# Kernel optimization log

Hardware: AMD Instinct MI355X
Metric: run time of the kernel (lower is better)

## Reference

```python
import jax, jax.numpy as jnp
import numpy as np

K = 3; PAD = 1; STRIDE = 1; EPS = 1e-5


def setup_inputs() -> dict:
    key = jax.random.key(0)
    k0, k1, k2 = jax.random.split(key, 3)
    B, C, H, W, O = 4, 256, 64, 64, 256
    x = jax.random.normal(k0, (B, C, H, W), jnp.float32)
    # offset conv: small random weights so offsets are nontrivial but bounded
    w_off = jax.random.normal(k1, (2 * K * K, C, K, K), jnp.float32) * 0.01
    b_off = jnp.zeros((2 * K * K,), jnp.float32)
    # kaiming normal, mode=fan_out: std = sqrt(2 / (O*K*K))
    w_def = jax.random.normal(k2, (O, C, K, K), jnp.float32) * np.float32(np.sqrt(2.0 / (O * K * K)))
    gamma = jnp.ones((O,), jnp.float32)
    beta = jnp.zeros((O,), jnp.float32)
    return {"x": x, "w_off": w_off, "b_off": b_off, "w_def": w_def, "gamma": gamma, "beta": beta}


def _bilinear_gather(x, py, px):
    """x: [B,C,H,W]; py,px: [B,K2,Ho,Wo] float sample coords.
    Returns [B,K2,Ho,Wo,C] with zero padding outside (per-corner masking,
    matching torchvision deform_conv2d)."""
    B, C, H, W = x.shape
    y0f = jnp.floor(py); x0f = jnp.floor(px)
    wy1 = py - y0f; wy0 = 1.0 - wy1
    wx1 = px - x0f; wx0 = 1.0 - wx1
    bidx = jnp.arange(B)[:, None, None, None]

    def corner(yf, xf, wgt):
        valid = (yf >= 0) & (yf <= H - 1) & (xf >= 0) & (xf <= W - 1)
        yc = jnp.clip(yf.astype(jnp.int32), 0, H - 1)
        xc = jnp.clip(xf.astype(jnp.int32), 0, W - 1)
        v = x[bidx, :, yc, xc]  # [B,K2,Ho,Wo,C] (advanced idx moves C last)
        return v * (wgt * valid)[..., None]

    return (corner(y0f, x0f, wy0 * wx0) + corner(y0f, x0f + 1.0, wy0 * wx1)
            + corner(y0f + 1.0, x0f, wy1 * wx0) + corner(y0f + 1.0, x0f + 1.0, wy1 * wx1))


def _forward(x, w_off, b_off, w_def, gamma, beta):
    B, C, H, W = x.shape
    O = w_def.shape[0]
    K2 = K * K
    # 1) offset-predicting conv
    off = jax.lax.conv_general_dilated(x, w_off, (STRIDE, STRIDE), ((PAD, PAD), (PAD, PAD)))
    off = off + b_off[None, :, None, None]
    Ho, Wo = off.shape[2], off.shape[3]
    off = off.reshape(B, K2, 2, Ho, Wo)  # pairs (dy, dx) per kernel tap
    # 2) deformable sampling locations
    ky, kx = jnp.meshgrid(jnp.arange(K, dtype=jnp.float32), jnp.arange(K, dtype=jnp.float32), indexing='ij')
    base_y = (jnp.arange(Ho, dtype=jnp.float32) * STRIDE - PAD)
    base_x = (jnp.arange(Wo, dtype=jnp.float32) * STRIDE - PAD)
    py = off[:, :, 0] + ky.reshape(K2)[None, :, None, None] + base_y[None, None, :, None]
    px = off[:, :, 1] + kx.reshape(K2)[None, :, None, None] + base_x[None, None, None, :]
    vals = _bilinear_gather(x, py, px)  # [B,K2,Ho,Wo,C]
    # 3) deform conv GEMM (bias=False)
    out = jnp.einsum('bkhwc,ock->bohw', vals, w_def.reshape(O, C, K2))
    # 4) BatchNorm (training mode: batch stats) + ReLU
    mean = out.mean(axis=(0, 2, 3))
    var = out.var(axis=(0, 2, 3))
    out = (out - mean[None, :, None, None]) * (gamma * jax.lax.rsqrt(var + EPS))[None, :, None, None]
    out = out + beta[None, :, None, None]
    return jax.nn.relu(out)


def reference(x, w_off, b_off, w_def, gamma, beta):
    return _forward(x, w_off, b_off, w_def, gamma, beta)
```

## Files before the change

### kernel.cpp

```cpp
#include <hip/hip_runtime.h>
#include <hip/hip_bf16.h>

typedef unsigned int  uint;
typedef unsigned short ushort;
typedef short bf16x8 __attribute__((ext_vector_type(8)));
typedef float f32x4  __attribute__((ext_vector_type(4)));

#define HW   4096
#define KD   2304

__device__ __forceinline__ void load_lds16(const void* g, void* l) {
    __builtin_amdgcn_global_load_lds((const __attribute__((address_space(1))) void*)g,
                                     (__attribute__((address_space(3))) void*)l, 16, 0, 0);
}
__device__ __forceinline__ float blo(uint u) { return __uint_as_float(u << 16); }
__device__ __forceinline__ float bhi(uint u) { return __uint_as_float(u & 0xffff0000u); }
__device__ __forceinline__ uint pack2(float e, float o) {
    __hip_bfloat16 he = __float2bfloat16(e), ho = __float2bfloat16(o);
    return (uint)(*(ushort*)&he) | ((uint)(*(ushort*)&ho) << 16);
}

__global__ void prep_x2(const float* __restrict__ x, uint* __restrict__ x2) {
    int idx = blockIdx.x * 256 + threadIdx.x;
    int a  = idx & 4095;
    int cp = (idx >> 12) & 127;
    int b  = idx >> 19;
    const float* p = x + ((size_t)(b * 256 + 2 * cp)) * HW + a;
    x2[idx] = pack2(p[0], p[HW]);
}

__global__ void prep_bt(const float* __restrict__ w_def, ushort* __restrict__ bt) {
    int idx = blockIdx.x * 256 + threadIdx.x;
    int c   = idx & 255;
    int tap = (idx >> 8) % 9;
    int o   = idx / KD;
    __hip_bfloat16 h = __float2bfloat16(w_def[(o * 256 + c) * 9 + tap]);
    bt[idx] = *(ushort*)&h;
}

__global__ void prep_bt0(const float* __restrict__ w_off, ushort* __restrict__ bt0) {
    int idx = blockIdx.x * 256 + threadIdx.x;
    int c   = idx & 255;
    int tap = (idx >> 8) % 9;
    int j   = idx / KD;
    float v = (j < 18) ? w_off[(j * 256 + c) * 9 + tap] : 0.f;
    __hip_bfloat16 h = __float2bfloat16(v);
    bt0[idx] = *(ushort*)&h;
}

__global__ __launch_bounds__(256) void gemm_off(const uint* __restrict__ x2,
                                                const ushort* __restrict__ bt0,
                                                const float* __restrict__ b_off,
                                                float* __restrict__ off) {
    int id = blockIdx.x;
    int xcd = id & 7;
    int b = xcd >> 1, h = (xcd & 1) * 32 + (id >> 3);
    int t = threadIdx.x, wv = t >> 6, lane = t & 63;
    int mrow = lane & 15, quad = lane >> 4;

    __shared__ uint   lX[3 * 32 * 64];
    __shared__ ushort lB[32 * 576];

    f32x4 acc[2];
    acc[0] = {0.f, 0.f, 0.f, 0.f};
    acc[1] = {0.f, 0.f, 0.f, 0.f};

    for (int cb = 0; cb < 4; ++cb) {
#pragma unroll
        for (int s = 0; s < 6; ++s) {
            int q  = s * 4 + wv;
            int dy = q >> 3;
            int y  = h + dy - 1;
            int dl = (q & 7) * 256 + lane * 4;
            int cp = dl >> 6, w4 = dl & 63;
            uint* dst = &lX[q * 256 + lane * 4];
            if ((unsigned)y < 64u) {
                const uint* src = x2 + ((size_t)(b * 128 + cb * 32 + cp)) * HW + y * 64 + w4;
                load_lds16(src, &lX[q * 256]);
            } else {
                uint4 z = {0u, 0u, 0u, 0u};
                *(uint4*)dst = z;
            }
        }
#pragma unroll
        for (int s = 0; s < 9; ++s) {
            int q = s * 4 + wv;
            int e = q * 512 + lane * 8;
            int o  = e / 576;
            int r  = e - o * 576;
            int chp = r >> 3;
            int ch  = chp ^ (o & 7);
            int tap = ch >> 3, k8 = ch & 7;
            const ushort* src = bt0 + (size_t)o * KD + tap * 256 + cb * 64 + k8 * 8;
            load_lds16(src, &lB[q * 512]);
        }
        __syncthreads();

#pragma unroll
        for (int tap = 0; tap < 9; ++tap) {
            int dy = tap / 3, dx = tap % 3;
            int xx = wv * 16 + mrow + dx - 1;
            bool vx = (unsigned)xx < 64u;
#pragma unroll
            for (int kb = 0; kb < 2; ++kb) {
                int cp0 = kb * 16 + quad * 4;
                uint ad[4];
#pragma unroll
                for (int i = 0; i < 4; ++i)
                    ad[i] = vx ? lX[(dy * 32 + cp0 + i) * 64 + xx] : 0u;
                bf16x8 af = *(bf16x8*)ad;
#pragma unroll
                for (int n = 0; n < 2; ++n) {
                    int o = n * 16 + mrow;
                    int chs = (tap * 8 + (((kb * 4 + quad)) ^ (o & 7)));
                    bf16x8 bfr = *(const bf16x8*)&lB[o * 576 + chs * 8];
                    acc[n] = __builtin_amdgcn_mfma_f32_16x16x32_bf16(af, bfr, acc[n], 0, 0, 0);
                }
            }
        }
        __syncthreads();
    }
#pragma unroll
    for (int n = 0; n < 2; ++n) {
        int o = n * 16 + mrow;
        float bias = (o < 18) ? b_off[o] : 0.f;
        f32x4 v = acc[n];
        v.x += bias; v.y += bias; v.z += bias; v.w += bias;
        int wpos = wv * 16 + quad * 4;
        *(f32x4*)(off + ((size_t)(b * 32 + o)) * HW + h * 64 + wpos) = v;
    }
}

__global__ __launch_bounds__(512) void fused_main(const uint* __restrict__ x2,
                                                  const ushort* __restrict__ bt,
                                                  const float* __restrict__ off,
                                                  float* __restrict__ out,
                                                  float* __restrict__ stats) {
    int id = blockIdx.x;
    int xcd = id & 7;
    int b = xcd >> 1, h = (xcd & 1) * 32 + (id >> 3);
    int t = threadIdx.x;
    int wv = t >> 6, lane = t & 63;
    int mrow = lane & 15, quad = lane >> 4;
    int w  = t & 63;
    int cq = (t >> 6) & 7;

    __shared__ int    sAc[4][9][64];
    __shared__ float  sWc[4][9][64];
    __shared__ ushort lA[2][64 * 64];
    __shared__ ushort lB[2][256 * 64];

    for (int i = t; i < 576; i += 512) {
        int tap = i >> 6, ww = i & 63;
        int hw = h * 64 + ww;
        float oy = off[((size_t)(b * 32 + 2 * tap)) * HW + hw];
        float ox = off[((size_t)(b * 32 + 2 * tap + 1)) * HW + hw];
        float py = oy + (float)(tap / 3 + h - 1);
        float px = ox + (float)(tap % 3 + ww - 1);
        float y0f = floorf(py), x0f = floorf(px);
        float wy1 = py - y0f, wx1 = px - x0f;
        float wy0 = 1.f - wy1, wx0 = 1.f - wx1;
        bool vy0 = (y0f >= 0.f) && (y0f <= 63.f);
        bool vy1 = (y0f >= -1.f) && (y0f <= 62.f);
        bool vx0 = (x0f >= 0.f) && (x0f <= 63.f);
        bool vx1 = (x0f >= -1.f) && (x0f <= 62.f);
        int iy0 = min(max((int)y0f, 0), 63),  iy1 = min(max((int)y0f + 1, 0), 63);
        int ix0 = min(max((int)x0f, 0), 63),  ix1 = min(max((int)x0f + 1, 0), 63);
        sAc[0][tap][ww] = iy0 * 64 + ix0;
        sAc[1][tap][ww] = iy0 * 64 + ix1;
        sAc[2][tap][ww] = iy1 * 64 + ix0;
        sAc[3][tap][ww] = iy1 * 64 + ix1;
        sWc[0][tap][ww] = wy0 * wx0 * (float)(vy0 && vx0);
        sWc[1][tap][ww] = wy0 * wx1 * (float)(vy0 && vx1);
        sWc[2][tap][ww] = wy1 * wx0 * (float)(vy1 && vx0);
        sWc[3][tap][ww] = wy1 * wx1 * (float)(vy1 && vx1);
    }
    __syncthreads();

    f32x4 acc[4][2];
#pragma unroll
    for (int m = 0; m < 4; ++m)
#pragma unroll
        for (int n = 0; n < 2; ++n) acc[m][n] = {0.f, 0.f, 0.f, 0.f};

    const uint* xb = x2 + (size_t)(b * 128) * HW;

    {
        int tap = 0, cb = 0;
        int a0 = sAc[0][tap][w], a1 = sAc[1][tap][w], a2 = sAc[2][tap][w], a3 = sAc[3][tap][w];
        float f0 = sWc[0][tap][w], f1 = sWc[1][tap][w], f2 = sWc[2][tap][w], f3 = sWc[3][tap][w];
        const uint* xp = xb + (size_t)(cb * 32 + cq * 4) * HW;
        uint r[4];
#pragma unroll
        for (int j = 0; j < 4; ++j) {
            const uint* p = xp + (size_t)j * HW;
            uint u0 = p[a0], u1 = p[a1], u2 = p[a2], u3 = p[a3];
            float e = f0 * blo(u0) + f1 * blo(u1) + f2 * blo(u2) + f3 * blo(u3);
            float o = f0 * bhi(u0) + f1 * bhi(u1) + f2 * bhi(u2) + f3 * bhi(u3);
            r[j] = pack2(e, o);
        }
        uint4 g = {r[0], r[1], r[2], r[3]};
        *(uint4*)&lA[0][w * 64 + ((cq ^ (w & 7)) * 8)] = g;
#pragma unroll
        for (int s2 = 0; s2 < 4; ++s2) {
            int e = s2 * 512 + t;
            int o = e >> 3, pp = e & 7;
            int k8 = pp ^ (o & 7);
            const ushort* src = bt + (size_t)o * KD + tap * 256 + cb * 64 + k8 * 8;
            load_lds16(src, &lB[0][(e & ~63) * 8]);
        }
    }

    int p = 0;
    for (int s = 0; s < 36; ++s) {
        __syncthreads();
        bool more = (s + 1) < 36;
        uint4 g;
        if (more) {
            int tap = (s + 1) >> 2, cb = (s + 1) & 3;
            int a0 = sAc[0][tap][w], a1 = sAc[1][tap][w], a2 = sAc[2][tap][w], a3 = sAc[3][tap][w];
            float f0 = sWc[0][tap][w], f1 = sWc[1][tap][w], f2 = sWc[2][tap][w], f3 = sWc[3][tap][w];
            const uint* xp = xb + (size_t)(cb * 32 + cq * 4) * HW;
            uint r[4];
#pragma unroll
            for (int j = 0; j < 4; ++j) {
                const uint* pq = xp + (size_t)j * HW;
                uint u0 = pq[a0], u1 = pq[a1], u2 = pq[a2], u3 = pq[a3];
                float e = f0 * blo(u0) + f1 * blo(u1) + f2 * blo(u2) + f3 * blo(u3);
                float o = f0 * bhi(u0) + f1 * bhi(u1) + f2 * bhi(u2) + f3 * bhi(u3);
                r[j] = pack2(e, o);
            }
            g = {r[0], r[1], r[2], r[3]};
#pragma unroll
            for (int s2 = 0; s2 < 4; ++s2) {
                int e = s2 * 512 + t;
                int o = e >> 3, pp = e & 7;
                int k8 = pp ^ (o & 7);
                const ushort* src = bt + (size_t)o * KD + tap * 256 + cb * 64 + k8 * 8;
                load_lds16(src, &lB[p ^ 1][(e & ~63) * 8]);
            }
        }
#pragma unroll
        for (int kb = 0; kb < 2; ++kb) {
            bf16x8 af[4];
#pragma unroll
            for (int m = 0; m < 4; ++m) {
                int r = m * 16 + mrow;
                af[m] = *(const bf16x8*)&lA[p][r * 64 + (((kb * 4 + quad) ^ (r & 7)) * 8)];
            }
#pragma unroll
            for (int n = 0; n < 2; ++n) {
                int r = wv * 32 + n * 16 + mrow;
                bf16x8 bfr = *(const bf16x8*)&lB[p][r * 64 + (((kb * 4 + quad) ^ (r & 7)) * 8)];
#pragma unroll
                for (int m = 0; m < 4; ++m)
                    acc[m][n] = __builtin_amdgcn_mfma_f32_16x16x32_bf16(af[m], bfr, acc[m][n], 0, 0, 0);
            }
        }
        if (more)
            *(uint4*)&lA[p ^ 1][w * 64 + ((cq ^ (w & 7)) * 8)] = g;
        p ^= 1;
    }

#pragma unroll
    for (int n = 0; n < 2; ++n) {
        int o = wv * 32 + n * 16 + mrow;
        float ss = 0.f, qq = 0.f;
#pragma unroll
        for (int m = 0; m < 4; ++m) {
            int pos = m * 16 + quad * 4;
            f32x4 v = acc[m][n];
            *(f32x4*)(out + ((size_t)(b * 256 + o)) * HW + h * 64 + pos) = v;
            ss += v.x + v.y + v.z + v.w;
            qq += v.x * v.x + v.y * v.y + v.z * v.z + v.w * v.w;
        }
        ss += __shfl_xor(ss, 16); ss += __shfl_xor(ss, 32);
        qq += __shfl_xor(qq, 16); qq += __shfl_xor(qq, 32);
        if (quad == 0) {
            atomicAdd(&stats[o], ss);
            atomicAdd(&stats[512 + o], qq);
        }
    }
}

__global__ void bn_finalize(const float* __restrict__ stats,
                            const float* __restrict__ gamma,
                            float* __restrict__ ms) {
    int o = threadIdx.x;
    float S = stats[o], S2 = stats[512 + o];
    float m  = S / 16384.f;
    float var = S2 / 16384.f - m * m;
    ms[o]       = m;
    ms[256 + o] = gamma[o] * rsqrtf(var + 1e-5f);
}

__global__ void bn_apply(float* __restrict__ out,
                         const float* __restrict__ ms,
                         const float* __restrict__ beta) {
    int idx4 = blockIdx.x * 256 + threadIdx.x;
    int o = (idx4 >> 10) & 255;
    float4 v = ((const float4*)out)[idx4];
    float mu = ms[o], sc = ms[256 + o], be = beta[o];
    v.x = fmaxf((v.x - mu) * sc + be, 0.f);
    v.y = fmaxf((v.y - mu) * sc + be, 0.f);
    v.z = fmaxf((v.z - mu) * sc + be, 0.f);
    v.w = fmaxf((v.w - mu) * sc + be, 0.f);
    ((float4*)out)[idx4] = v;
}

extern "C" void kernel_launch(void* const* d_in, const int* in_sizes, int n_in,
                              void* d_out, int out_size, void* d_ws, size_t ws_size,
                              hipStream_t stream) {
    const float* x     = (const float*)d_in[0];
    const float* w_off = (const float*)d_in[1];
    const float* b_off = (const float*)d_in[2];
    const float* w_def = (const float*)d_in[3];
    const float* gamma = (const float*)d_in[4];
    const float* beta  = (const float*)d_in[5];
    float* out = (float*)d_out;

    char* ws = (char*)d_ws;
    uint*   x2    = (uint*)ws;
    ushort* bt    = (ushort*)(ws + 8388608);
    ushort* bt0   = (ushort*)(ws + 9568256);
    float*  off   = (float*)(ws + 9715712);
    float*  stats = (float*)(ws + 11812864);
    float*  ms    = (float*)(ws + 11816960);

    hipMemsetAsync(stats, 0, 4096, stream);
    prep_x2 <<<8192, 256, 0, stream>>>(x, x2);
    prep_bt <<<2304, 256, 0, stream>>>(w_def, bt);
    prep_bt0<<<288,  256, 0, stream>>>(w_off, bt0);
    gemm_off<<<256, 256, 0, stream>>>(x2, bt0, b_off, off);
    fused_main<<<256, 512, 0, stream>>>(x2, bt, off, out, stats);
    bn_finalize<<<1, 256, 0, stream>>>(stats, gamma, ms);
    bn_apply<<<4096, 256, 0, stream>>>(out, ms, beta);
}
```

Measured before the change: 176.0 us.

## Fuse offset conv, deform GEMM and BatchNorm into one persistent kernel

Merges the three prep kernels into one launch. The offset conv, deformable GEMM and BatchNorm+ReLU now run in a single kernel that uses a grid-wide atomic counter barrier, so the offset tensor and the pre-BN output no longer round-trip through global memory. Waves are split into producer/consumer roles: four waves do bilinear gathering and B-tile loads while four waves issue MFMA over a 64x256 tile, instead of all waves doing both. Correctness of the spin barrier depends on all 256 blocks being co-resident, and idle waves during the offset conv reduce utilization there.

```diff
diff --git a/kernel.cpp b/kernel.cpp
--- a/kernel.cpp
+++ b/kernel.cpp
@@ -6,8 +6,8 @@
 typedef short bf16x8 __attribute__((ext_vector_type(8)));
 typedef float f32x4  __attribute__((ext_vector_type(4)));
 
-#define HW   4096
-#define KD   2304
+#define HW 4096
+#define KD 2304
 
 __device__ __forceinline__ void load_lds16(const void* g, void* l) {
     __builtin_amdgcn_global_load_lds((const __attribute__((address_space(1))) void*)g,
@@ -20,143 +20,160 @@
     return (uint)(*(ushort*)&he) | ((uint)(*(ushort*)&ho) << 16);
 }
 
-__global__ void prep_x2(const float* __restrict__ x, uint* __restrict__ x2) {
-    int idx = blockIdx.x * 256 + threadIdx.x;
-    int a  = idx & 4095;
-    int cp = (idx >> 12) & 127;
-    int b  = idx >> 19;
-    const float* p = x + ((size_t)(b * 256 + 2 * cp)) * HW + a;
-    x2[idx] = pack2(p[0], p[HW]);
-}
-
-__global__ void prep_bt(const float* __restrict__ w_def, ushort* __restrict__ bt) {
-    int idx = blockIdx.x * 256 + threadIdx.x;
-    int c   = idx & 255;
-    int tap = (idx >> 8) % 9;
-    int o   = idx / KD;
-    __hip_bfloat16 h = __float2bfloat16(w_def[(o * 256 + c) * 9 + tap]);
-    bt[idx] = *(ushort*)&h;
-}
-
-__global__ void prep_bt0(const float* __restrict__ w_off, ushort* __restrict__ bt0) {
-    int idx = blockIdx.x * 256 + threadIdx.x;
-    int c   = idx & 255;
-    int tap = (idx >> 8) % 9;
-    int j   = idx / KD;
-    float v = (j < 18) ? w_off[(j * 256 + c) * 9 + tap] : 0.f;
-    __hip_bfloat16 h = __float2bfloat16(v);
-    bt0[idx] = *(ushort*)&h;
-}
-
-__global__ __launch_bounds__(256) void gemm_off(const uint* __restrict__ x2,
-                                                const ushort* __restrict__ bt0,
-                                                const float* __restrict__ b_off,
-                                                float* __restrict__ off) {
-    int id = blockIdx.x;
-    int xcd = id & 7;
-    int b = xcd >> 1, h = (xcd & 1) * 32 + (id >> 3);
-    int t = threadIdx.x, wv = t >> 6, lane = t & 63;
-    int mrow = lane & 15, quad = lane >> 4;
-
-    __shared__ uint   lX[3 * 32 * 64];
-    __shared__ ushort lB[32 * 576];
-
-    f32x4 acc[2];
-    acc[0] = {0.f, 0.f, 0.f, 0.f};
-    acc[1] = {0.f, 0.f, 0.f, 0.f};
-
-    for (int cb = 0; cb < 4; ++cb) {
-#pragma unroll
-        for (int s = 0; s < 6; ++s) {
-            int q  = s * 4 + wv;
-            int dy = q >> 3;
-            int y  = h + dy - 1;
-            int dl = (q & 7) * 256 + lane * 4;
-            int cp = dl >> 6, w4 = dl & 63;
-            uint* dst = &lX[q * 256 + lane * 4];
-            if ((unsigned)y < 64u) {
-                const uint* src = x2 + ((size_t)(b * 128 + cb * 32 + cp)) * HW + y * 64 + w4;
-                load_lds16(src, &lX[q * 256]);
-            } else {
-                uint4 z = {0u, 0u, 0u, 0u};
-                *(uint4*)dst = z;
-            }
-        }
-#pragma unroll
-        for (int s = 0; s < 9; ++s) {
-            int q = s * 4 + wv;
-            int e = q * 512 + lane * 8;
-            int o  = e / 576;
-            int r  = e - o * 576;
-            int chp = r >> 3;
-            int ch  = chp ^ (o & 7);
-            int tap = ch >> 3, k8 = ch & 7;
-            const ushort* src = bt0 + (size_t)o * KD + tap * 256 + cb * 64 + k8 * 8;
-            load_lds16(src, &lB[q * 512]);
-        }
-        __syncthreads();
-
-#pragma unroll
-        for (int tap = 0; tap < 9; ++tap) {
-            int dy = tap / 3, dx = tap % 3;
-            int xx = wv * 16 + mrow + dx - 1;
-            bool vx = (unsigned)xx < 64u;
-#pragma unroll
-            for (int kb = 0; kb < 2; ++kb) {
-                int cp0 = kb * 16 + quad * 4;
-                uint ad[4];
-#pragma unroll
-                for (int i = 0; i < 4; ++i)
-                    ad[i] = vx ? lX[(dy * 32 + cp0 + i) * 64 + xx] : 0u;
-                bf16x8 af = *(bf16x8*)ad;
-#pragma unroll
-                for (int n = 0; n < 2; ++n) {
-                    int o = n * 16 + mrow;
-                    int chs = (tap * 8 + (((kb * 4 + quad)) ^ (o & 7)));
-                    bf16x8 bfr = *(const bf16x8*)&lB[o * 576 + chs * 8];
-                    acc[n] = __builtin_amdgcn_mfma_f32_16x16x32_bf16(af, bfr, acc[n], 0, 0, 0);
-                }
-            }
-        }
-        __syncthreads();
-    }
-#pragma unroll
-    for (int n = 0; n < 2; ++n) {
-        int o = n * 16 + mrow;
-        float bias = (o < 18) ? b_off[o] : 0.f;
-        f32x4 v = acc[n];
-        v.x += bias; v.y += bias; v.z += bias; v.w += bias;
-        int wpos = wv * 16 + quad * 4;
-        *(f32x4*)(off + ((size_t)(b * 32 + o)) * HW + h * 64 + wpos) = v;
-    }
-}
-
-__global__ __launch_bounds__(512) void fused_main(const uint* __restrict__ x2,
-                                                  const ushort* __restrict__ bt,
-                                                  const float* __restrict__ off,
-                                                  float* __restrict__ out,
-                                                  float* __restrict__ stats) {
+__global__ void prep_all(const float* __restrict__ x, const float* __restrict__ w_def,
+                         const float* __restrict__ w_off,
+                         uint* __restrict__ x2, ushort* __restrict__ bt,
+                         ushort* __restrict__ bt0) {
+    int gid = blockIdx.x, t = threadIdx.x;
+    if (gid < 8192) {
+        int idx = gid * 256 + t;
+        int a  = idx & 4095;
+        int cp = (idx >> 12) & 127;
+        int b  = idx >> 19;
+        const float* p = x + ((size_t)(b * 256 + 2 * cp)) * HW + a;
+        x2[idx] = pack2(p[0], p[HW]);
+    } else if (gid < 10496) {
+        int idx = (gid - 8192) * 256 + t;
+        int c   = idx & 255;
+        int tap = (idx >> 8) % 9;
+        int o   = idx / KD;
+        __hip_bfloat16 h = __float2bfloat16(w_def[(o * 256 + c) * 9 + tap]);
+        bt[idx] = *(ushort*)&h;
+    } else {
+        int idx = (gid - 10496) * 256 + t;
+        int c   = idx & 255;
+        int tap = (idx >> 8) % 9;
+        int j   = idx / KD;
+        float v = (j < 18) ? w_off[(j * 256 + c) * 9 + tap] : 0.f;
+        __hip_bfloat16 h = __float2bfloat16(v);
+        bt0[idx] = *(ushort*)&h;
+    }
+}
+
+__global__ __launch_bounds__(512, 4) void fused_all(
+        const uint* __restrict__ x2, const ushort* __restrict__ bt,
+        const ushort* __restrict__ bt0, const float* __restrict__ b_off,
+        const float* __restrict__ gamma, const float* __restrict__ beta,
+        float* __restrict__ out, float* __restrict__ stats, uint* __restrict__ counter) {
     int id = blockIdx.x;
     int xcd = id & 7;
     int b = xcd >> 1, h = (xcd & 1) * 32 + (id >> 3);
     int t = threadIdx.x;
     int wv = t >> 6, lane = t & 63;
     int mrow = lane & 15, quad = lane >> 4;
-    int w  = t & 63;
-    int cq = (t >> 6) & 7;
-
-    __shared__ int    sAc[4][9][64];
-    __shared__ float  sWc[4][9][64];
-    __shared__ ushort lA[2][64 * 64];
-    __shared__ ushort lB[2][256 * 64];
-
-    for (int i = t; i < 576; i += 512) {
-        int tap = i >> 6, ww = i & 63;
-        int hw = h * 64 + ww;
-        float oy = off[((size_t)(b * 32 + 2 * tap)) * HW + hw];
-        float ox = off[((size_t)(b * 32 + 2 * tap + 1)) * HW + hw];
+
+    __shared__ __align__(16) char smem[81920];
+    uint*   lX   = (uint*)smem;
+    ushort* lB0  = (ushort*)(smem + 24576);
+    float*  sOff = (float*)smem;
+    ushort* lAb  = (ushort*)smem;
+    ushort* lBb  = (ushort*)(smem + 16384);
+
+    f32x4 acc0[2];
+    acc0[0] = {0.f, 0.f, 0.f, 0.f};
+    acc0[1] = {0.f, 0.f, 0.f, 0.f};
+    for (int cb = 0; cb < 4; ++cb) {
+#pragma unroll
+        for (int s = 0; s < 3; ++s) {
+            int q  = s * 8 + wv;
+            int dy = q >> 3;
+            int y  = h + dy - 1;
+            int dl = (q & 7) * 256 + lane * 4;
+            int cp = dl >> 6, w4 = dl & 63;
+            if ((unsigned)y < 64u) {
+                const uint* src = x2 + ((size_t)(b * 128 + cb * 32 + cp)) * HW + y * 64 + w4;
+                load_lds16(src, &lX[q * 256]);
+            } else {
+                uint4 z = {0u, 0u, 0u, 0u};
+                *(uint4*)&lX[q * 256 + lane * 4] = z;
+            }
+        }
+#pragma unroll
+        for (int s = 0; s < 5; ++s) {
+            int q = s * 8 + wv;
+            if (q < 36) {
+                int e = q * 512 + lane * 8;
+                int o  = e / 576;
+                int r  = e - o * 576;
+                int chp = r >> 3;
+                int ch  = chp ^ (o & 7);
+                int tap = ch >> 3, k8 = ch & 7;
+                const ushort* src = bt0 + (size_t)o * KD + tap * 256 + cb * 64 + k8 * 8;
+                load_lds16(src, &lB0[q * 512]);
+            }
+        }
+        __syncthreads();
+        if (wv < 4) {
+#pragma unroll
+            for (int tap = 0; tap < 9; ++tap) {
+                int dy = tap / 3, dx = tap % 3;
+                int xx = wv * 16 + mrow + dx - 1;
+                bool vx = (unsigned)xx < 64u;
+#pragma unroll
+                for (int kb = 0; kb < 2; ++kb) {
+                    int cp0 = kb * 16 + quad * 4;
+                    uint ad[4];
+#pragma unroll
+                    for (int i = 0; i < 4; ++i)
+                        ad[i] = vx ? lX[(dy * 32 + cp0 + i) * 64 + xx] : 0u;
+                    bf16x8 af = *(bf16x8*)ad;
+#pragma unroll
+                    for (int n = 0; n < 2; ++n) {
+                        int o = n * 16 + mrow;
+                        int chs = tap * 8 + ((kb * 4 + quad) ^ (o & 7));
+                        bf16x8 bfr = *(const bf16x8*)&lB0[o * 576 + chs * 8];
+                        acc0[n] = __builtin_amdgcn_mfma_f32_16x16x32_bf16(af, bfr, acc0[n], 0, 0, 0);
+                    }
+                }
+            }
+        }
+        __syncthreads();
+    }
+    if (wv < 4) {
+#pragma unroll
+        for (int n = 0; n < 2; ++n) {
+            int j = n * 16 + mrow;
+            if (j < 18) {
+                float bias = b_off[j];
+                f32x4 v = acc0[n];
+                v.x += bias; v.y += bias; v.z += bias; v.w += bias;
+                *(f32x4*)&sOff[j * 64 + wv * 16 + quad * 4] = v;
+            }
+        }
+    }
+    __syncthreads();
+
+    int pw = t & 63;
+    int cq = (t >> 6) & 3;
+    float oy0=0,oy1=0,oy2=0,oy3=0,oy4=0,oy5=0,oy6=0,oy7=0,oy8=0;
+    float ox0=0,ox1=0,ox2=0,ox3=0,ox4=0,ox5=0,ox6=0,ox7=0,ox8=0;
+    if (wv >= 4) {
+        oy0 = sOff[ 0*64+pw]; ox0 = sOff[ 1*64+pw];
+        oy1 = sOff[ 2*64+pw]; ox1 = sOff[ 3*64+pw];
+        oy2 = sOff[ 4*64+pw]; ox2 = sOff[ 5*64+pw];
+        oy3 = sOff[ 6*64+pw]; ox3 = sOff[ 7*64+pw];
+        oy4 = sOff[ 8*64+pw]; ox4 = sOff[ 9*64+pw];
+        oy5 = sOff[10*64+pw]; ox5 = sOff[11*64+pw];
+        oy6 = sOff[12*64+pw]; ox6 = sOff[13*64+pw];
+        oy7 = sOff[14*64+pw]; ox7 = sOff[15*64+pw];
+        oy8 = sOff[16*64+pw]; ox8 = sOff[17*64+pw];
+    }
+    __syncthreads();
+
+    int a0=0,a1=0,a2=0,a3=0;
+    float f0=0,f1=0,f2=0,f3=0;
+
+    auto coords = [&](int tap) {
+        float oy, ox;
+        switch (tap) {
+            case 0: oy=oy0; ox=ox0; break;  case 1: oy=oy1; ox=ox1; break;
+            case 2: oy=oy2; ox=ox2; break;  case 3: oy=oy3; ox=ox3; break;
+            case 4: oy=oy4; ox=ox4; break;  case 5: oy=oy5; ox=ox5; break;
+            case 6: oy=oy6; ox=ox6; break;  case 7: oy=oy7; ox=ox7; break;
+            default: oy=oy8; ox=ox8; break;
+        }
         float py = oy + (float)(tap / 3 + h - 1);
-        float px = ox + (float)(tap % 3 + ww - 1);
+        float px = ox + (float)(tap % 3 + pw - 1);
         float y0f = floorf(py), x0f = floorf(px);
         float wy1 = py - y0f, wx1 = px - x0f;
         float wy0 = 1.f - wy1, wx0 = 1.f - wx1;
@@ -166,146 +183,135 @@
         bool vx1 = (x0f >= -1.f) && (x0f <= 62.f);
         int iy0 = min(max((int)y0f, 0), 63),  iy1 = min(max((int)y0f + 1, 0), 63);
         int ix0 = min(max((int)x0f, 0), 63),  ix1 = min(max((int)x0f + 1, 0), 63);
-        sAc[0][tap][ww] = iy0 * 64 + ix0;
-        sAc[1][tap][ww] = iy0 * 64 + ix1;
-        sAc[2][tap][ww] = iy1 * 64 + ix0;
-        sAc[3][tap][ww] = iy1 * 64 + ix1;
-        sWc[0][tap][ww] = wy0 * wx0 * (float)(vy0 && vx0);
-        sWc[1][tap][ww] = wy0 * wx1 * (float)(vy0 && vx1);
-        sWc[2][tap][ww] = wy1 * wx0 * (float)(vy1 && vx0);
-        sWc[3][tap][ww] = wy1 * wx1 * (float)(vy1 && vx1);
-    }
-    __syncthreads();
-
-    f32x4 acc[4][2];
-#pragma unroll
-    for (int m = 0; m < 4; ++m)
-#pragma unroll
-        for (int n = 0; n < 2; ++n) acc[m][n] = {0.f, 0.f, 0.f, 0.f};
-
-    const uint* xb = x2 + (size_t)(b * 128) * HW;
-
-    {
-        int tap = 0, cb = 0;
-        int a0 = sAc[0][tap][w], a1 = sAc[1][tap][w], a2 = sAc[2][tap][w], a3 = sAc[3][tap][w];
-        float f0 = sWc[0][tap][w], f1 = sWc[1][tap][w], f2 = sWc[2][tap][w], f3 = sWc[3][tap][w];
-        const uint* xp = xb + (size_t)(cb * 32 + cq * 4) * HW;
-        uint r[4];
-#pragma unroll
-        for (int j = 0; j < 4; ++j) {
+        a0 = iy0 * 64 + ix0; a1 = iy0 * 64 + ix1;
+        a2 = iy1 * 64 + ix0; a3 = iy1 * 64 + ix1;
+        f0 = wy0 * wx0 * (float)(vy0 && vx0);
+        f1 = wy0 * wx1 * (float)(vy0 && vx1);
+        f2 = wy1 * wx0 * (float)(vy1 && vx0);
+        f3 = wy1 * wx1 * (float)(vy1 && vx1);
+    };
+
+    auto stage = [&](int s, int buf) {
+        int tap = s >> 2, cb = s & 3;
+        const uint* xp = x2 + ((size_t)(b * 128 + cb * 32 + cq * 8)) * HW;
+        uint r[8];
+#pragma unroll
+        for (int j = 0; j < 8; ++j) {
             const uint* p = xp + (size_t)j * HW;
             uint u0 = p[a0], u1 = p[a1], u2 = p[a2], u3 = p[a3];
             float e = f0 * blo(u0) + f1 * blo(u1) + f2 * blo(u2) + f3 * blo(u3);
             float o = f0 * bhi(u0) + f1 * bhi(u1) + f2 * bhi(u2) + f3 * bhi(u3);
             r[j] = pack2(e, o);
         }
-        uint4 g = {r[0], r[1], r[2], r[3]};
-        *(uint4*)&lA[0][w * 64 + ((cq ^ (w & 7)) * 8)] = g;
-#pragma unroll
-        for (int s2 = 0; s2 < 4; ++s2) {
-            int e = s2 * 512 + t;
-            int o = e >> 3, pp = e & 7;
-            int k8 = pp ^ (o & 7);
-            const ushort* src = bt + (size_t)o * KD + tap * 256 + cb * 64 + k8 * 8;
-            load_lds16(src, &lB[0][(e & ~63) * 8]);
-        }
-    }
-
-    int p = 0;
+        ushort* lA = lAb + buf * 4096;
+        *(uint4*)&lA[pw * 64 + (((cq * 2)     ^ (pw & 7)) * 8)] = *(uint4*)&r[0];
+        *(uint4*)&lA[pw * 64 + (((cq * 2 + 1) ^ (pw & 7)) * 8)] = *(uint4*)&r[4];
+        ushort* lB = lBb + buf * 16384;
+        int pt = t - 256;
+#pragma unroll
+        for (int s2 = 0; s2 < 8; ++s2) {
+            int e2 = s2 * 256 + pt;
+            int o2 = e2 >> 3, pp = e2 & 7;
+            int k8 = pp ^ (o2 & 7);
+            const ushort* src = bt + (size_t)o2 * KD + tap * 256 + cb * 64 + k8 * 8;
+            load_lds16(src, &lB[(e2 & ~63) * 8]);
+        }
+    };
+
+    f32x4 acc[4][4];
+    if (wv < 4) {
+#pragma unroll
+        for (int m = 0; m < 4; ++m)
+#pragma unroll
+            for (int n = 0; n < 4; ++n) acc[m][n] = {0.f, 0.f, 0.f, 0.f};
+    } else {
+        coords(0);
+        stage(0, 0);
+    }
+
+    int buf = 0;
     for (int s = 0; s < 36; ++s) {
         __syncthreads();
-        bool more = (s + 1) < 36;
-        uint4 g;
-        if (more) {
-            int tap = (s + 1) >> 2, cb = (s + 1) & 3;
-            int a0 = sAc[0][tap][w], a1 = sAc[1][tap][w], a2 = sAc[2][tap][w], a3 = sAc[3][tap][w];
-            float f0 = sWc[0][tap][w], f1 = sWc[1][tap][w], f2 = sWc[2][tap][w], f3 = sWc[3][tap][w];
-            const uint* xp = xb + (size_t)(cb * 32 + cq * 4) * HW;
-            uint r[4];
-#pragma unroll
-            for (int j = 0; j < 4; ++j) {
-                const uint* pq = xp + (size_t)j * HW;
-                uint u0 = pq[a0], u1 = pq[a1], u2 = pq[a2], u3 = pq[a3];
-                float e = f0 * blo(u0) + f1 * blo(u1) + f2 * blo(u2) + f3 * blo(u3);
-                float o = f0 * bhi(u0) + f1 * bhi(u1) + f2 * bhi(u2) + f3 * bhi(u3);
-                r[j] = pack2(e, o);
-            }
-            g = {r[0], r[1], r[2], r[3]};
-#pragma unroll
-            for (int s2 = 0; s2 < 4; ++s2) {
-                int e = s2 * 512 + t;
-                int o = e >> 3, pp = e & 7;
-                int k8 = pp ^ (o & 7);
-                const ushort* src = bt + (size_t)o * KD + tap * 256 + cb * 64 + k8 * 8;
-                load_lds16(src, &lB[p ^ 1][(e & ~63) * 8]);
-            }
-        }
-#pragma unroll
-        for (int kb = 0; kb < 2; ++kb) {
-            bf16x8 af[4];
+        if (wv >= 4) {
+            int sn = s + 1;
+            if (sn < 36) {
+                if ((sn & 3) == 0) coords(sn >> 2);
+                stage(sn, buf ^ 1);
+            }
+        } else {
+            ushort* lA = lAb + buf * 4096;
+            ushort* lB = lBb + buf * 16384;
+#pragma unroll
+            for (int kb = 0; kb < 2; ++kb) {
+                bf16x8 af[4];
+#pragma unroll
+                for (int m = 0; m < 4; ++m) {
+                    int r = m * 16 + mrow;
+                    af[m] = *(const bf16x8*)&lA[r * 64 + (((kb * 4 + quad) ^ (r & 7)) * 8)];
+                }
+#pragma unroll
+                for (int n = 0; n < 4; ++n) {
+                    int r = wv * 64 + n * 16 + mrow;
+                    bf16x8 bfr = *(const bf16x8*)&lB[r * 64 + (((kb * 4 + quad) ^ (r & 7)) * 8)];
+#pragma unroll
+                    for (int m = 0; m < 4; ++m)
+                        acc[m][n] = __builtin_amdgcn_mfma_f32_16x16x32_bf16(af[m], bfr, acc[m][n], 0, 0, 0);
+                }
+            }
+        }
+        buf ^= 1;
+    }
+
+    if (wv < 4) {
+#pragma unroll
+        for (int n = 0; n < 4; ++n) {
+            int o = wv * 64 + n * 16 + mrow;
+            float ss = 0.f, qq = 0.f;
 #pragma unroll
             for (int m = 0; m < 4; ++m) {
-                int r = m * 16 + mrow;
-                af[m] = *(const bf16x8*)&lA[p][r * 64 + (((kb * 4 + quad) ^ (r & 7)) * 8)];
-            }
-#pragma unroll
-            for (int n = 0; n < 2; ++n) {
-                int r = wv * 32 + n * 16 + mrow;
-                bf16x8 bfr = *(const bf16x8*)&lB[p][r * 64 + (((kb * 4 + quad) ^ (r & 7)) * 8)];
-#pragma unroll
-                for (int m = 0; m < 4; ++m)
-                    acc[m][n] = __builtin_amdgcn_mfma_f32_16x16x32_bf16(af[m], bfr, acc[m][n], 0, 0, 0);
-            }
-        }
-        if (more)
-            *(uint4*)&lA[p ^ 1][w * 64 + ((cq ^ (w & 7)) * 8)] = g;
-        p ^= 1;
-    }
-
-#pragma unroll
-    for (int n = 0; n < 2; ++n) {
-        int o = wv * 32 + n * 16 + mrow;
-        float ss = 0.f, qq = 0.f;
-#pragma unroll
-        for (int m = 0; m < 4; ++m) {
-            int pos = m * 16 + quad * 4;
-            f32x4 v = acc[m][n];
-            *(f32x4*)(out + ((size_t)(b * 256 + o)) * HW + h * 64 + pos) = v;
-            ss += v.x + v.y + v.z + v.w;
-            qq += v.x * v.x + v.y * v.y + v.z * v.z + v.w * v.w;
-        }
-        ss += __shfl_xor(ss, 16); ss += __shfl_xor(ss, 32);
-        qq += __shfl_xor(qq, 16); qq += __shfl_xor(qq, 32);
-        if (quad == 0) {
-            atomicAdd(&stats[o], ss);
-            atomicAdd(&stats[512 + o], qq);
-        }
-    }
-}
-
-__global__ void bn_finalize(const float* __restrict__ stats,
-                            const float* __restrict__ gamma,
-                            float* __restrict__ ms) {
-    int o = threadIdx.x;
-    float S = stats[o], S2 = stats[512 + o];
-    float m  = S / 16384.f;
-    float var = S2 / 16384.f - m * m;
-    ms[o]       = m;
-    ms[256 + o] = gamma[o] * rsqrtf(var + 1e-5f);
-}
-
-__global__ void bn_apply(float* __restrict__ out,
-                         const float* __restrict__ ms,
-                         const float* __restrict__ beta) {
-    int idx4 = blockIdx.x * 256 + threadIdx.x;
-    int o = (idx4 >> 10) & 255;
-    float4 v = ((const float4*)out)[idx4];
-    float mu = ms[o], sc = ms[256 + o], be = beta[o];
-    v.x = fmaxf((v.x - mu) * sc + be, 0.f);
-    v.y = fmaxf((v.y - mu) * sc + be, 0.f);
-    v.z = fmaxf((v.z - mu) * sc + be, 0.f);
-    v.w = fmaxf((v.w - mu) * sc + be, 0.f);
-    ((float4*)out)[idx4] = v;
+                f32x4 v = acc[m][n];
+                ss += v.x + v.y + v.z + v.w;
+                qq += v.x * v.x + v.y * v.y + v.z * v.z + v.w * v.w;
+            }
+            ss += __shfl_xor(ss, 16); ss += __shfl_xor(ss, 32);
+            qq += __shfl_xor(qq, 16); qq += __shfl_xor(qq, 32);
+            if (quad == 0) {
+                atomicAdd(&stats[o], ss);
+                atomicAdd(&stats[512 + o], qq);
+            }
+        }
+    }
+    __threadfence();
+    __syncthreads();
+    if (t == 0) {
+        __hip_atomic_fetch_add(counter, 1u, __ATOMIC_ACQ_REL, __HIP_MEMORY_SCOPE_AGENT);
+        while (__hip_atomic_load(counter, __ATOMIC_ACQUIRE, __HIP_MEMORY_SCOPE_AGENT) < 256u) {
+            __builtin_amdgcn_s_sleep(2);
+        }
+    }
+    __syncthreads();
+
+    if (wv < 4) {
+#pragma unroll
+        for (int n = 0; n < 4; ++n) {
+            int o = wv * 64 + n * 16 + mrow;
+            float S  = __hip_atomic_load(&stats[o],       __ATOMIC_RELAXED, __HIP_MEMORY_SCOPE_AGENT);
+            float S2 = __hip_atomic_load(&stats[512 + o], __ATOMIC_RELAXED, __HIP_MEMORY_SCOPE_AGENT);
+            float mean = S * (1.f / 16384.f);
+            float var  = S2 * (1.f / 16384.f) - mean * mean;
+            float sc = gamma[o] * rsqrtf(var + 1e-5f);
+            float be = beta[o];
+#pragma unroll
+            for (int m = 0; m < 4; ++m) {
+                f32x4 v = acc[m][n];
+                v.x = fmaxf((v.x - mean) * sc + be, 0.f);
+                v.y = fmaxf((v.y - mean) * sc + be, 0.f);
+                v.z = fmaxf((v.z - mean) * sc + be, 0.f);
+                v.w = fmaxf((v.w - mean) * sc + be, 0.f);
+                *(f32x4*)(out + ((size_t)(b * 256 + o)) * HW + h * 64 + m * 16 + quad * 4) = v;
+            }
+        }
+    }
 }
 
 extern "C" void kernel_launch(void* const* d_in, const int* in_sizes, int n_in,
@@ -323,16 +329,10 @@
     uint*   x2    = (uint*)ws;
     ushort* bt    = (ushort*)(ws + 8388608);
     ushort* bt0   = (ushort*)(ws + 9568256);
-    float*  off   = (float*)(ws + 9715712);
-    float*  stats = (float*)(ws + 11812864);
-    float*  ms    = (float*)(ws + 11816960);
-
-    hipMemsetAsync(stats, 0, 4096, stream);
-    prep_x2 <<<8192, 256, 0, stream>>>(x, x2);
-    prep_bt <<<2304, 256, 0, stream>>>(w_def, bt);
-    prep_bt0<<<288,  256, 0, stream>>>(w_off, bt0);
-    gemm_off<<<256, 256, 0, stream>>>(x2, bt0, b_off, off);
-    fused_main<<<256, 512, 0, stream>>>(x2, bt, off, out, stats);
-    bn_finalize<<<1, 256, 0, stream>>>(stats, gamma, ms);
-    bn_apply<<<4096, 256, 0, stream>>>(out, ms, beta);
-}
+    float*  stats = (float*)(ws + 9715712);
+    uint*   counter = (uint*)(ws + 9715712 + 4096);
+
+    hipMemsetAsync(stats, 0, 4224, stream);
+    prep_all<<<10784, 256, 0, stream>>>(x, w_def, w_off, x2, bt, bt0);
+    fused_all<<<256, 512, 0, stream>>>(x2, bt, bt0, b_off, gamma, beta, out, stats, counter);
+}
```

New measurement: 298.9 us. 69.8% more time.
